# Kernel optimization log

Hardware: AMD Instinct MI355X
Metric: run time of the kernel (lower is better)

Reference implementation:

```python
import jax, jax.numpy as jnp
import numpy as np

D_MODEL = 1024
N_HEADS = 16
HEAD_DIM = D_MODEL // N_HEADS


def setup_inputs() -> dict:
    key = jax.random.key(0)
    ks = jax.random.split(key, 5)
    scale = 1.0 / np.sqrt(D_MODEL)
    return {
        "x": jax.random.normal(ks[0], (4, 2048, D_MODEL), dtype=jnp.float32),
        "W_q": jax.random.normal(ks[1], (D_MODEL, D_MODEL), dtype=jnp.float32) * scale,
        "W_k": jax.random.normal(ks[2], (D_MODEL, D_MODEL), dtype=jnp.float32) * scale,
        "W_v": jax.random.normal(ks[3], (D_MODEL, D_MODEL), dtype=jnp.float32) * scale,
        "W_o": jax.random.normal(ks[4], (D_MODEL, D_MODEL), dtype=jnp.float32) * scale,
    }


def _split_heads(t):
    # (B, T, d_model) -> (B, H, T, head_dim)
    B, T, _ = t.shape
    return t.reshape(B, T, N_HEADS, HEAD_DIM).transpose(0, 2, 1, 3)


def reference(x, W_q, W_k, W_v, W_o):
    B, T, _ = x.shape
    # torch nn.Linear: y = x @ W.T
    q = _split_heads(x @ W_q.T)
    k = _split_heads(x @ W_k.T)
    v = _split_heads(x @ W_v.T)
    scale = jnp.asarray(np.sqrt(HEAD_DIM), x.dtype)
    # (B, H, T, T) scores, additive causal mask (triu above diagonal = -inf)
    scores = jnp.einsum("bhqd,bhkd->bhqk", q, k) / scale
    causal = jnp.tril(jnp.ones((T, T), dtype=bool))
    scores = jnp.where(causal, scores, jnp.asarray(-jnp.inf, scores.dtype))
    weights = jax.nn.softmax(scores, axis=-1)
    out = jnp.einsum("bhqk,bhkd->bhqd", weights, v)
    out = out.transpose(0, 2, 1, 3).reshape(B, T, D_MODEL)
    out = out @ W_o.T
    return out, k, v
```

## Files before the change

### kernel.cpp

```cpp
#include <hip/hip_runtime.h>
#include <stdint.h>

typedef __bf16 bf16;
typedef __bf16 bf16x8 __attribute__((ext_vector_type(8)));
typedef __bf16 bf16x4 __attribute__((ext_vector_type(4)));
typedef short short4v __attribute__((ext_vector_type(4)));
typedef float f32x4 __attribute__((ext_vector_type(4)));
typedef uint32_t u32;

#define MFMA_BF16(a, b, c) __builtin_amdgcn_mfma_f32_16x16x32_bf16(a, b, c, 0, 0, 0)
#define MFMA16(a, b, c)                                                   \
  __builtin_amdgcn_mfma_f32_16x16x16bf16_1k(*(const short4v*)&(a),        \
                                            *(const short4v*)&(b), c, 0, 0, 0)

constexpr int D_MODEL = 1024;
constexpr int T_SEQ = 2048;
constexpr int NH = 16;
constexpr int HD = 64;
constexpr size_t OUT_ELEMS = (size_t)4 * T_SEQ * D_MODEL;
constexpr size_t X_ELEMS = OUT_ELEMS;
constexpr size_t W_ELEMS = (size_t)D_MODEL * D_MODEL;

__device__ __forceinline__ void gload16(const bf16* g, bf16* l) {
  __builtin_amdgcn_global_load_lds(
      (const __attribute__((address_space(1))) unsigned int*)g,
      (__attribute__((address_space(3))) unsigned int*)l, 16, 0, 0);
}

__global__ __launch_bounds__(256) void convert_kernel(
    const float* __restrict__ x, const float* __restrict__ wq,
    const float* __restrict__ wk, const float* __restrict__ wv,
    bf16* __restrict__ dst) {
  const size_t nchunk = (X_ELEMS + 3 * W_ELEMS) / 8;
  for (size_t c = (size_t)blockIdx.x * 256 + threadIdx.x; c < nchunk;
       c += (size_t)gridDim.x * 256) {
    const size_t off = c * 8;
    const float* src;
    size_t rel;
    if (off < X_ELEMS) {
      src = x;
      rel = off;
    } else {
      const size_t j = off - X_ELEMS;
      const int w = (int)(j >> 20);
      rel = j & (W_ELEMS - 1);
      src = (w == 0) ? wq : (w == 1) ? wk : wv;
    }
    const f32x4 a = *(const f32x4*)(src + rel);
    const f32x4 b = *(const f32x4*)(src + rel + 4);
    bf16x8 o;
#pragma unroll
    for (int e = 0; e < 4; ++e) {
      o[e] = (bf16)a[e];
      o[e + 4] = (bf16)b[e];
    }
    *(bf16x8*)(dst + off) = o;
  }
}

template <bool B_F32>
__global__ __launch_bounds__(256) void gemm2(
    const bf16* __restrict__ A, const bf16* __restrict__ WB,
    const float* __restrict__ WF, int modeBase, bf16* __restrict__ dstB,
    float* __restrict__ dstF1, float* __restrict__ dstF2) {
  const int z = blockIdx.z;
  const int mode = modeBase + z;
  const bf16* Bb = B_F32 ? nullptr : WB + (size_t)z * W_ELEMS;
  const int m0 = blockIdx.y * 128, n0 = blockIdx.x * 128;
  const int tid = threadIdx.x;
  const int wave = tid >> 6, lane = tid & 63;
  const int quad = lane >> 4, c16 = lane & 15;
  const int wr = wave >> 1, wc = wave & 1;

  __shared__ __align__(16) bf16 As[128 * 32];
  __shared__ __align__(16) bf16 Bs[128 * 32];

  f32x4 acc[4][4];
#pragma unroll
  for (int i = 0; i < 4; ++i)
#pragma unroll
    for (int j = 0; j < 4; ++j) acc[i][j] = (f32x4){0.f, 0.f, 0.f, 0.f};

  const int rIn = lane >> 2;
  const int kgo = (lane & 3) * 8;
  const int rA0 = wave * 16 + rIn;
  const int rA1 = (wave + 4) * 16 + rIn;

  for (int k0 = 0; k0 < 1024; k0 += 32) {
    __syncthreads();
    gload16(A + (size_t)(m0 + rA0) * 1024 + k0 + kgo, &As[wave * 512]);
    gload16(A + (size_t)(m0 + rA1) * 1024 + k0 + kgo, &As[(wave + 4) * 512]);
    if (!B_F32) {
      gload16(Bb + (size_t)(n0 + rA0) * 1024 + k0 + kgo, &Bs[wave * 512]);
      gload16(Bb + (size_t)(n0 + rA1) * 1024 + k0 + kgo, &Bs[(wave + 4) * 512]);
    } else {
#pragma unroll
      for (int p = 0; p < 2; ++p) {
        const int slot = p * 256 + tid;
        const int row = slot >> 2, kg = slot & 3;
        const float* bp = WF + (size_t)(n0 + row) * 1024 + k0 + kg * 8;
        const f32x4 b0 = *(const f32x4*)bp;
        const f32x4 b1 = *(const f32x4*)(bp + 4);
        bf16x8 vb;
#pragma unroll
        for (int e = 0; e < 4; ++e) {
          vb[e] = (bf16)b0[e];
          vb[e + 4] = (bf16)b1[e];
        }
        *(bf16x8*)&Bs[(size_t)slot * 8] = vb;
      }
    }
    asm volatile("s_waitcnt vmcnt(0)" ::: "memory");
    __syncthreads();

    const bf16x8* Av = (const bf16x8*)As;
    const bf16x8* Bv = (const bf16x8*)Bs;
    bf16x8 af[4], bfr[4];
#pragma unroll
    for (int i = 0; i < 4; ++i) af[i] = Av[(wr * 64 + i * 16 + c16) * 4 + quad];
#pragma unroll
    for (int j = 0; j < 4; ++j) bfr[j] = Bv[(wc * 64 + j * 16 + c16) * 4 + quad];
#pragma unroll
    for (int i = 0; i < 4; ++i)
#pragma unroll
      for (int j = 0; j < 4; ++j) acc[i][j] = MFMA_BF16(af[i], bfr[j], acc[i][j]);
  }

  const int row0 = m0 + wr * 64, col0 = n0 + wc * 64;
#pragma unroll
  for (int i = 0; i < 4; ++i) {
#pragma unroll
    for (int r = 0; r < 4; ++r) {
      const int row = row0 + i * 16 + quad * 4 + r;
      const int b = row >> 11, t = row & 2047;
#pragma unroll
      for (int j = 0; j < 4; ++j) {
        const int cc = col0 + j * 16 + c16;
        const float v = acc[i][j][r];
        if (mode == 0) {
          dstB[(size_t)row * 1024 + cc] = (bf16)v;
        } else if (mode == 3) {
          dstF1[(size_t)row * 1024 + cc] = v;
        } else {
          const int h = cc >> 6, d = cc & 63;
          float* df = (mode == 1) ? dstF1 : dstF2;
          df[((size_t)(b * NH + h) * T_SEQ + t) * HD + d] = v;
        }
      }
    }
  }
}

__device__ __forceinline__ void load_kv(const float* Kg, const float* Vg,
                                        int t0, int st, int sd,
                                        f32x4 pk[2][2], f32x4 pv[2][2]) {
#pragma unroll
  for (int p = 0; p < 2; ++p) {
    const float* kp = Kg + (size_t)(t0 + p * 32 + st) * HD + sd * 8;
    pk[p][0] = *(const f32x4*)kp;
    pk[p][1] = *(const f32x4*)(kp + 4);
    const float* vp = Vg + (size_t)(t0 + p * 32 + st) * HD + sd * 8;
    pv[p][0] = *(const f32x4*)vp;
    pv[p][1] = *(const f32x4*)(vp + 4);
  }
}

__global__ __launch_bounds__(256, 4) void attn_kernel(
    const bf16* __restrict__ Q, const float* __restrict__ K,
    const float* __restrict__ V, bf16* __restrict__ Aout) {
  const int bx = blockIdx.x;
  const int by = blockIdx.y;
  const int r16 = (bx + ((by >> 4) << 2)) & 15;
  const int qt = (r16 < 8) ? r16 : 23 - r16;
  const int bh = by;
  const int b = bh >> 4, h = bh & 15;
  const int tid = threadIdx.x, wave = tid >> 6, lane = tid & 63;
  const int quad = lane >> 4, c16 = lane & 15;

  __shared__ __align__(16) bf16 Ks[64 * 70];
  __shared__ __align__(16) bf16 Vs[64 * 70];

  const int q0w = qt * 128 + wave * 32;
  const bf16* Qb = Q + ((size_t)b * T_SEQ + q0w) * D_MODEL + h * HD;
  const float* Kg = K + (size_t)bh * T_SEQ * HD;
  const float* Vg = V + (size_t)bh * T_SEQ * HD;

  bf16x8 aq[2][2];
#pragma unroll
  for (int mt = 0; mt < 2; ++mt) {
    const bf16* qp = Qb + (size_t)(mt * 16 + c16) * D_MODEL + quad * 8;
    aq[mt][0] = *(const bf16x8*)qp;
    aq[mt][1] = *(const bf16x8*)(qp + 32);
  }

  f32x4 O[2][4], racc[2];
#pragma unroll
  for (int mt = 0; mt < 2; ++mt) {
    racc[mt] = (f32x4){0.f, 0.f, 0.f, 0.f};
#pragma unroll
    for (int dj = 0; dj < 4; ++dj) O[mt][dj] = (f32x4){0.f, 0.f, 0.f, 0.f};
  }

  bf16x4 ones4;
#pragma unroll
  for (int e = 0; e < 4; ++e) ones4[e] = (bf16)1.0f;

  const float sc = 0.125f * 1.44269504088896340736f;
  const int nkt = 2 * qt + 2;
  const int st = tid >> 3, sd = tid & 7;

  f32x4 pk[2][2], pv[2][2];
  load_kv(Kg, Vg, 0, st, sd, pk, pv);

  for (int kt = 0; kt < nkt; ++kt) {
    const int t0 = kt * 64;

    __syncthreads();
#pragma unroll
    for (int p = 0; p < 2; ++p) {
      const int t = p * 32 + st;
      bf16x8 kb;
#pragma unroll
      for (int e = 0; e < 4; ++e) {
        kb[e] = (bf16)pk[p][0][e];
        kb[e + 4] = (bf16)pk[p][1][e];
      }
      *(bf16x8*)&Ks[t * 70 + sd * 8] = kb;
#pragma unroll
      for (int e = 0; e < 4; ++e) {
        Vs[(sd * 8 + e) * 70 + t] = (bf16)pv[p][0][e];
        Vs[(sd * 8 + 4 + e) * 70 + t] = (bf16)pv[p][1][e];
      }
    }
    if (kt + 1 < nkt) load_kv(Kg, Vg, t0 + 64, st, sd, pk, pv);
    __syncthreads();

    const bool act[2] = {t0 <= q0w + 15, t0 <= q0w + 31};

    bf16x4 ap16[2][4];
#pragma unroll
    for (int j = 0; j < 4; ++j) {
      const bf16* kp = &Ks[(j * 16 + c16) * 70 + quad * 8];
      const bf16x8 ak0 = *(const bf16x8*)kp;
      const bf16x8 ak1 = *(const bf16x8*)(kp + 32);
#pragma unroll
      for (int mt = 0; mt < 2; ++mt) {
        if (!act[mt]) continue;
        f32x4 s = (f32x4){0.f, 0.f, 0.f, 0.f};
        s = MFMA_BF16(ak0, aq[mt][0], s);
        s = MFMA_BF16(ak1, aq[mt][1], s);
        const int trow = t0 + j * 16 + quad * 4;
        const int qcol = q0w + mt * 16 + c16;
        bf16x4 pa;
#pragma unroll
        for (int r = 0; r < 4; ++r)
          pa[r] = (bf16)((trow + r <= qcol) ? exp2f(s[r] * sc) : 0.f);
        ap16[mt][j] = pa;
      }
    }

    if (act[1]) {
#pragma unroll
      for (int mt = 0; mt < 2; ++mt) {
        if (!act[mt]) continue;
#pragma unroll
        for (int j = 0; j < 4; ++j)
          racc[mt] = MFMA16(ap16[mt][j], ones4, racc[mt]);
      }
#pragma unroll
      for (int dj = 0; dj < 4; ++dj) {
#pragma unroll
        for (int j = 0; j < 4; ++j) {
          const int a = (dj * 16 + c16) * 70 + j * 16 + quad * 4;
          bf16x4 bv;
          *(u32*)&bv = *(const u32*)&Vs[a];
          *((u32*)&bv + 1) = *(const u32*)&Vs[a + 2];
#pragma unroll
          for (int mt = 0; mt < 2; ++mt) {
            if (!act[mt]) continue;
            O[mt][dj] = MFMA16(ap16[mt][j], bv, O[mt][dj]);
          }
        }
      }
    }
  }

#pragma unroll
  for (int mt = 0; mt < 2; ++mt) {
    f32x4 inv;
#pragma unroll
    for (int r = 0; r < 4; ++r) inv[r] = 1.f / racc[mt][r];
#pragma unroll
    for (int dj = 0; dj < 4; ++dj)
#pragma unroll
      for (int r = 0; r < 4; ++r) {
        const int q = q0w + mt * 16 + quad * 4 + r;
        Aout[((size_t)b * T_SEQ + q) * D_MODEL + h * HD + dj * 16 + c16] =
            (bf16)(O[mt][dj][r] * inv[r]);
      }
  }
}

extern "C" void kernel_launch(void* const* d_in, const int* in_sizes, int n_in,
                              void* d_out, int out_size, void* d_ws, size_t ws_size,
                              hipStream_t stream) {
  const float* x = (const float*)d_in[0];
  const float* wq = (const float*)d_in[1];
  const float* wk = (const float*)d_in[2];
  const float* wv = (const float*)d_in[3];
  const float* wo = (const float*)d_in[4];

  float* out = (float*)d_out;
  float* kout = out + OUT_ELEMS;
  float* vout = out + 2 * OUT_ELEMS;

  bf16* ws = (bf16*)d_ws;
  bf16* Qbuf = ws;
  bf16* Abuf = ws;

  bf16* cvt = (bf16*)d_out;
  const bf16* xb = cvt;
  const bf16* wb = cvt + X_ELEMS;

  convert_kernel<<<dim3(2048), 256, 0, stream>>>(x, wq, wk, wv, cvt);
  gemm2<false><<<dim3(8, 64, 3), 256, 0, stream>>>(xb, wb, nullptr, 0, Qbuf,
                                                   kout, vout);
  attn_kernel<<<dim3(16, 64), 256, 0, stream>>>(Qbuf, kout, vout, Abuf);
  gemm2<true><<<dim3(8, 64, 1), 256, 0, stream>>>(Abuf, nullptr, wo, 3,
                                                  nullptr, out, nullptr);
}
```

Baseline: 436.7 us.

## Use 8 waves per attention block and pre-convert W_o to bf16

The attention kernel now runs 512 threads per block with each wave owning 16 query rows instead of 32. That halves per-wave register state and spreads the causal work more finely, while each thread loads one K/V row instead of two. Separately, W_o is converted to bf16 into the workspace when it has room, so the output projection can use the bf16-B GEMM path. The cost is an extra conversion launch, and each K/V tile is now shared by more waves.

```diff
diff --git a/kernel.cpp b/kernel.cpp
--- a/kernel.cpp
+++ b/kernel.cpp
@@ -58,6 +58,24 @@
   }
 }
 
+__global__ __launch_bounds__(256) void convert_wo(const float* __restrict__ wo,
+                                                  bf16* __restrict__ dst) {
+  const size_t nchunk = W_ELEMS / 8;
+  for (size_t c = (size_t)blockIdx.x * 256 + threadIdx.x; c < nchunk;
+       c += (size_t)gridDim.x * 256) {
+    const size_t off = c * 8;
+    const f32x4 a = *(const f32x4*)(wo + off);
+    const f32x4 b = *(const f32x4*)(wo + off + 4);
+    bf16x8 o;
+#pragma unroll
+    for (int e = 0; e < 4; ++e) {
+      o[e] = (bf16)a[e];
+      o[e + 4] = (bf16)b[e];
+    }
+    *(bf16x8*)(dst + off) = o;
+  }
+}
+
 template <bool B_F32>
 __global__ __launch_bounds__(256) void gemm2(
     const bf16* __restrict__ A, const bf16* __restrict__ WB,
@@ -152,54 +170,45 @@
 }
 
 __device__ __forceinline__ void load_kv(const float* Kg, const float* Vg,
-                                        int t0, int st, int sd,
-                                        f32x4 pk[2][2], f32x4 pv[2][2]) {
-#pragma unroll
-  for (int p = 0; p < 2; ++p) {
-    const float* kp = Kg + (size_t)(t0 + p * 32 + st) * HD + sd * 8;
-    pk[p][0] = *(const f32x4*)kp;
-    pk[p][1] = *(const f32x4*)(kp + 4);
-    const float* vp = Vg + (size_t)(t0 + p * 32 + st) * HD + sd * 8;
-    pv[p][0] = *(const f32x4*)vp;
-    pv[p][1] = *(const f32x4*)(vp + 4);
-  }
-}
-
-__global__ __launch_bounds__(256, 4) void attn_kernel(
+                                        int t0, int st, int sd, f32x4 pk[2],
+                                        f32x4 pv[2]) {
+  const float* kp = Kg + (size_t)(t0 + st) * HD + sd * 8;
+  pk[0] = *(const f32x4*)kp;
+  pk[1] = *(const f32x4*)(kp + 4);
+  const float* vp = Vg + (size_t)(t0 + st) * HD + sd * 8;
+  pv[0] = *(const f32x4*)vp;
+  pv[1] = *(const f32x4*)(vp + 4);
+}
+
+__global__ __launch_bounds__(512, 8) void attn_kernel(
     const bf16* __restrict__ Q, const float* __restrict__ K,
     const float* __restrict__ V, bf16* __restrict__ Aout) {
   const int bx = blockIdx.x;
   const int by = blockIdx.y;
   const int r16 = (bx + ((by >> 4) << 2)) & 15;
   const int qt = (r16 < 8) ? r16 : 23 - r16;
-  const int bh = by;
-  const int b = bh >> 4, h = bh & 15;
+  const int b = by >> 4, h = by & 15;
   const int tid = threadIdx.x, wave = tid >> 6, lane = tid & 63;
   const int quad = lane >> 4, c16 = lane & 15;
 
   __shared__ __align__(16) bf16 Ks[64 * 70];
   __shared__ __align__(16) bf16 Vs[64 * 70];
 
-  const int q0w = qt * 128 + wave * 32;
+  const int q0w = qt * 128 + wave * 16;
   const bf16* Qb = Q + ((size_t)b * T_SEQ + q0w) * D_MODEL + h * HD;
-  const float* Kg = K + (size_t)bh * T_SEQ * HD;
-  const float* Vg = V + (size_t)bh * T_SEQ * HD;
-
-  bf16x8 aq[2][2];
-#pragma unroll
-  for (int mt = 0; mt < 2; ++mt) {
-    const bf16* qp = Qb + (size_t)(mt * 16 + c16) * D_MODEL + quad * 8;
-    aq[mt][0] = *(const bf16x8*)qp;
-    aq[mt][1] = *(const bf16x8*)(qp + 32);
-  }
-
-  f32x4 O[2][4], racc[2];
-#pragma unroll
-  for (int mt = 0; mt < 2; ++mt) {
-    racc[mt] = (f32x4){0.f, 0.f, 0.f, 0.f};
-#pragma unroll
-    for (int dj = 0; dj < 4; ++dj) O[mt][dj] = (f32x4){0.f, 0.f, 0.f, 0.f};
-  }
+  const float* Kg = K + (size_t)by * T_SEQ * HD;
+  const float* Vg = V + (size_t)by * T_SEQ * HD;
+
+  bf16x8 aq[2];
+  {
+    const bf16* qp = Qb + (size_t)c16 * D_MODEL + quad * 8;
+    aq[0] = *(const bf16x8*)qp;
+    aq[1] = *(const bf16x8*)(qp + 32);
+  }
+
+  f32x4 O[4], racc = (f32x4){0.f, 0.f, 0.f, 0.f};
+#pragma unroll
+  for (int dj = 0; dj < 4; ++dj) O[dj] = (f32x4){0.f, 0.f, 0.f, 0.f};
 
   bf16x4 ones4;
 #pragma unroll
@@ -209,64 +218,52 @@
   const int nkt = 2 * qt + 2;
   const int st = tid >> 3, sd = tid & 7;
 
-  f32x4 pk[2][2], pv[2][2];
+  f32x4 pk[2], pv[2];
   load_kv(Kg, Vg, 0, st, sd, pk, pv);
 
   for (int kt = 0; kt < nkt; ++kt) {
     const int t0 = kt * 64;
 
     __syncthreads();
-#pragma unroll
-    for (int p = 0; p < 2; ++p) {
-      const int t = p * 32 + st;
+    {
       bf16x8 kb;
 #pragma unroll
       for (int e = 0; e < 4; ++e) {
-        kb[e] = (bf16)pk[p][0][e];
-        kb[e + 4] = (bf16)pk[p][1][e];
-      }
-      *(bf16x8*)&Ks[t * 70 + sd * 8] = kb;
+        kb[e] = (bf16)pk[0][e];
+        kb[e + 4] = (bf16)pk[1][e];
+      }
+      *(bf16x8*)&Ks[st * 70 + sd * 8] = kb;
 #pragma unroll
       for (int e = 0; e < 4; ++e) {
-        Vs[(sd * 8 + e) * 70 + t] = (bf16)pv[p][0][e];
-        Vs[(sd * 8 + 4 + e) * 70 + t] = (bf16)pv[p][1][e];
+        Vs[(sd * 8 + e) * 70 + st] = (bf16)pv[0][e];
+        Vs[(sd * 8 + 4 + e) * 70 + st] = (bf16)pv[1][e];
       }
     }
     if (kt + 1 < nkt) load_kv(Kg, Vg, t0 + 64, st, sd, pk, pv);
     __syncthreads();
 
-    const bool act[2] = {t0 <= q0w + 15, t0 <= q0w + 31};
-
-    bf16x4 ap16[2][4];
-#pragma unroll
-    for (int j = 0; j < 4; ++j) {
-      const bf16* kp = &Ks[(j * 16 + c16) * 70 + quad * 8];
-      const bf16x8 ak0 = *(const bf16x8*)kp;
-      const bf16x8 ak1 = *(const bf16x8*)(kp + 32);
-#pragma unroll
-      for (int mt = 0; mt < 2; ++mt) {
-        if (!act[mt]) continue;
+    const bool act = t0 <= q0w + 15;
+
+    bf16x4 ap16[4];
+    if (act) {
+#pragma unroll
+      for (int j = 0; j < 4; ++j) {
+        const bf16* kp = &Ks[(j * 16 + c16) * 70 + quad * 8];
+        const bf16x8 ak0 = *(const bf16x8*)kp;
+        const bf16x8 ak1 = *(const bf16x8*)(kp + 32);
         f32x4 s = (f32x4){0.f, 0.f, 0.f, 0.f};
-        s = MFMA_BF16(ak0, aq[mt][0], s);
-        s = MFMA_BF16(ak1, aq[mt][1], s);
+        s = MFMA_BF16(ak0, aq[0], s);
+        s = MFMA_BF16(ak1, aq[1], s);
         const int trow = t0 + j * 16 + quad * 4;
-        const int qcol = q0w + mt * 16 + c16;
+        const int qcol = q0w + c16;
         bf16x4 pa;
 #pragma unroll
         for (int r = 0; r < 4; ++r)
           pa[r] = (bf16)((trow + r <= qcol) ? exp2f(s[r] * sc) : 0.f);
-        ap16[mt][j] = pa;
-      }
-    }
-
-    if (act[1]) {
-#pragma unroll
-      for (int mt = 0; mt < 2; ++mt) {
-        if (!act[mt]) continue;
-#pragma unroll
-        for (int j = 0; j < 4; ++j)
-          racc[mt] = MFMA16(ap16[mt][j], ones4, racc[mt]);
-      }
+        ap16[j] = pa;
+      }
+#pragma unroll
+      for (int j = 0; j < 4; ++j) racc = MFMA16(ap16[j], ones4, racc);
 #pragma unroll
       for (int dj = 0; dj < 4; ++dj) {
 #pragma unroll
@@ -275,30 +272,23 @@
           bf16x4 bv;
           *(u32*)&bv = *(const u32*)&Vs[a];
           *((u32*)&bv + 1) = *(const u32*)&Vs[a + 2];
-#pragma unroll
-          for (int mt = 0; mt < 2; ++mt) {
-            if (!act[mt]) continue;
-            O[mt][dj] = MFMA16(ap16[mt][j], bv, O[mt][dj]);
-          }
+          O[dj] = MFMA16(ap16[j], bv, O[dj]);
         }
       }
     }
   }
 
-#pragma unroll
-  for (int mt = 0; mt < 2; ++mt) {
-    f32x4 inv;
-#pragma unroll
-    for (int r = 0; r < 4; ++r) inv[r] = 1.f / racc[mt][r];
-#pragma unroll
-    for (int dj = 0; dj < 4; ++dj)
-#pragma unroll
-      for (int r = 0; r < 4; ++r) {
-        const int q = q0w + mt * 16 + quad * 4 + r;
-        Aout[((size_t)b * T_SEQ + q) * D_MODEL + h * HD + dj * 16 + c16] =
-            (bf16)(O[mt][dj][r] * inv[r]);
-      }
-  }
+  f32x4 inv;
+#pragma unroll
+  for (int r = 0; r < 4; ++r) inv[r] = 1.f / racc[r];
+#pragma unroll
+  for (int dj = 0; dj < 4; ++dj)
+#pragma unroll
+    for (int r = 0; r < 4; ++r) {
+      const int q = q0w + quad * 4 + r;
+      Aout[((size_t)b * T_SEQ + q) * D_MODEL + h * HD + dj * 16 + c16] =
+          (bf16)(O[dj][r] * inv[r]);
+    }
 }
 
 extern "C" void kernel_launch(void* const* d_in, const int* in_sizes, int n_in,
@@ -322,10 +312,19 @@
   const bf16* xb = cvt;
   const bf16* wb = cvt + X_ELEMS;
 
+  const bool wo_bf = ws_size >= (X_ELEMS + W_ELEMS) * sizeof(bf16);
+  bf16* wo_b = ws + X_ELEMS;
+
   convert_kernel<<<dim3(2048), 256, 0, stream>>>(x, wq, wk, wv, cvt);
+  if (wo_bf) convert_wo<<<dim3(512), 256, 0, stream>>>(wo, wo_b);
   gemm2<false><<<dim3(8, 64, 3), 256, 0, stream>>>(xb, wb, nullptr, 0, Qbuf,
                                                    kout, vout);
-  attn_kernel<<<dim3(16, 64), 256, 0, stream>>>(Qbuf, kout, vout, Abuf);
-  gemm2<true><<<dim3(8, 64, 1), 256, 0, stream>>>(Abuf, nullptr, wo, 3,
-                                                  nullptr, out, nullptr);
-}
+  attn_kernel<<<dim3(16, 64), 512, 0, stream>>>(Qbuf, kout, vout, Abuf);
+  if (wo_bf) {
+    gemm2<false><<<dim3(8, 64, 1), 256, 0, stream>>>(Abuf, wo_b, nullptr, 3,
+                                                     nullptr, out, nullptr);
+  } else {
+    gemm2<true><<<dim3(8, 64, 1), 256, 0, stream>>>(Abuf, nullptr, wo, 3,
+                                                    nullptr, out, nullptr);
+  }
+}
```

Measured after the change: 499.4 us. 1.14x slower.

## Use ds_read_b64_tr_b16 for V operand and pre-convert W_o to bf16

Applied to the files above, without the earlier changes.

The V tile is now stored in LDS in a 16x16-blocked row layout with vectorized 16-byte writes, replacing scalar transposed stores. The PV MFMA B operands are read with the hardware transpose-read instruction ds_read_b64_tr_b16. A separate kernel converts W_o to bf16 in workspace so the output projection can use the bf16-B GEMM path instead of converting fp32 weights inside the GEMM. This adds an extra launch and relies on the workspace being large enough; it falls back to the old path otherwise.

```diff
diff --git a/kernel.cpp b/kernel.cpp
--- a/kernel.cpp
+++ b/kernel.cpp
@@ -6,12 +6,18 @@
 typedef __bf16 bf16x4 __attribute__((ext_vector_type(4)));
 typedef short short4v __attribute__((ext_vector_type(4)));
 typedef float f32x4 __attribute__((ext_vector_type(4)));
+typedef int v2i __attribute__((ext_vector_type(2)));
 typedef uint32_t u32;
 
 #define MFMA_BF16(a, b, c) __builtin_amdgcn_mfma_f32_16x16x32_bf16(a, b, c, 0, 0, 0)
 #define MFMA16(a, b, c)                                                   \
   __builtin_amdgcn_mfma_f32_16x16x16bf16_1k(*(const short4v*)&(a),        \
                                             *(const short4v*)&(b), c, 0, 0, 0)
+
+#define TRREAD(dst, va, IMM)                                             \
+  asm volatile("ds_read_b64_tr_b16 %0, %1 offset:" #IMM                  \
+               : "=v"(dst)                                               \
+               : "v"(va))
 
 constexpr int D_MODEL = 1024;
 constexpr int T_SEQ = 2048;
@@ -58,6 +64,24 @@
   }
 }
 
+__global__ __launch_bounds__(256) void convert_wo(const float* __restrict__ wo,
+                                                  bf16* __restrict__ dst) {
+  const size_t nchunk = W_ELEMS / 8;
+  for (size_t c = (size_t)blockIdx.x * 256 + threadIdx.x; c < nchunk;
+       c += (size_t)gridDim.x * 256) {
+    const size_t off = c * 8;
+    const f32x4 a = *(const f32x4*)(wo + off);
+    const f32x4 b = *(const f32x4*)(wo + off + 4);
+    bf16x8 o;
+#pragma unroll
+    for (int e = 0; e < 4; ++e) {
+      o[e] = (bf16)a[e];
+      o[e + 4] = (bf16)b[e];
+    }
+    *(bf16x8*)(dst + off) = o;
+  }
+}
+
 template <bool B_F32>
 __global__ __launch_bounds__(256) void gemm2(
     const bf16* __restrict__ A, const bf16* __restrict__ WB,
@@ -172,18 +196,17 @@
   const int by = blockIdx.y;
   const int r16 = (bx + ((by >> 4) << 2)) & 15;
   const int qt = (r16 < 8) ? r16 : 23 - r16;
-  const int bh = by;
-  const int b = bh >> 4, h = bh & 15;
+  const int b = by >> 4, h = by & 15;
   const int tid = threadIdx.x, wave = tid >> 6, lane = tid & 63;
   const int quad = lane >> 4, c16 = lane & 15;
 
   __shared__ __align__(16) bf16 Ks[64 * 70];
-  __shared__ __align__(16) bf16 Vs[64 * 70];
+  __shared__ __align__(16) bf16 Vs[4096];
 
   const int q0w = qt * 128 + wave * 32;
   const bf16* Qb = Q + ((size_t)b * T_SEQ + q0w) * D_MODEL + h * HD;
-  const float* Kg = K + (size_t)bh * T_SEQ * HD;
-  const float* Vg = V + (size_t)bh * T_SEQ * HD;
+  const float* Kg = K + (size_t)by * T_SEQ * HD;
+  const float* Vg = V + (size_t)by * T_SEQ * HD;
 
   bf16x8 aq[2][2];
 #pragma unroll
@@ -208,6 +231,9 @@
   const float sc = 0.125f * 1.44269504088896340736f;
   const int nkt = 2 * qt + 2;
   const int st = tid >> 3, sd = tid & 7;
+  const u32 vtr =
+      (u32)(uintptr_t)(const __attribute__((address_space(3))) bf16*)Vs +
+      (u32)lane * 8;
 
   f32x4 pk[2][2], pv[2][2];
   load_kv(Kg, Vg, 0, st, sd, pk, pv);
@@ -219,18 +245,17 @@
 #pragma unroll
     for (int p = 0; p < 2; ++p) {
       const int t = p * 32 + st;
-      bf16x8 kb;
+      bf16x8 kb, vb;
 #pragma unroll
       for (int e = 0; e < 4; ++e) {
         kb[e] = (bf16)pk[p][0][e];
         kb[e + 4] = (bf16)pk[p][1][e];
+        vb[e] = (bf16)pv[p][0][e];
+        vb[e + 4] = (bf16)pv[p][1][e];
       }
       *(bf16x8*)&Ks[t * 70 + sd * 8] = kb;
-#pragma unroll
-      for (int e = 0; e < 4; ++e) {
-        Vs[(sd * 8 + e) * 70 + t] = (bf16)pv[p][0][e];
-        Vs[(sd * 8 + 4 + e) * 70 + t] = (bf16)pv[p][1][e];
-      }
+      *(bf16x8*)&Vs[(((t >> 4) * 4 + (sd >> 1)) * 256) + (t & 15) * 16 +
+                    (sd & 1) * 8] = vb;
     }
     if (kt + 1 < nkt) load_kv(Kg, Vg, t0 + 64, st, sd, pk, pv);
     __syncthreads();
@@ -267,21 +292,29 @@
         for (int j = 0; j < 4; ++j)
           racc[mt] = MFMA16(ap16[mt][j], ones4, racc[mt]);
       }
-#pragma unroll
-      for (int dj = 0; dj < 4; ++dj) {
-#pragma unroll
-        for (int j = 0; j < 4; ++j) {
-          const int a = (dj * 16 + c16) * 70 + j * 16 + quad * 4;
-          bf16x4 bv;
-          *(u32*)&bv = *(const u32*)&Vs[a];
-          *((u32*)&bv + 1) = *(const u32*)&Vs[a + 2];
-#pragma unroll
-          for (int mt = 0; mt < 2; ++mt) {
-            if (!act[mt]) continue;
-            O[mt][dj] = MFMA16(ap16[mt][j], bv, O[mt][dj]);
-          }
-        }
-      }
+      v2i bv0, bv1, bv2, bv3;
+#define PV_DJ(DJ, O0, O1, O2, O3)                                        \
+  {                                                                      \
+    TRREAD(bv0, vtr, O0);                                                \
+    TRREAD(bv1, vtr, O1);                                                \
+    TRREAD(bv2, vtr, O2);                                                \
+    TRREAD(bv3, vtr, O3);                                                \
+    asm volatile("s_waitcnt lgkmcnt(0)" ::: "memory");                   \
+    __builtin_amdgcn_sched_barrier(0);                                   \
+    _Pragma("unroll") for (int mt = 0; mt < 2; ++mt) {                   \
+      if (act[mt]) {                                                     \
+        O[mt][DJ] = MFMA16(ap16[mt][0], bv0, O[mt][DJ]);                 \
+        O[mt][DJ] = MFMA16(ap16[mt][1], bv1, O[mt][DJ]);                 \
+        O[mt][DJ] = MFMA16(ap16[mt][2], bv2, O[mt][DJ]);                 \
+        O[mt][DJ] = MFMA16(ap16[mt][3], bv3, O[mt][DJ]);                 \
+      }                                                                  \
+    }                                                                    \
+  }
+      PV_DJ(0, 0, 2048, 4096, 6144)
+      PV_DJ(1, 512, 2560, 4608, 6656)
+      PV_DJ(2, 1024, 3072, 5120, 7168)
+      PV_DJ(3, 1536, 3584, 5632, 7680)
+#undef PV_DJ
     }
   }
 
@@ -322,10 +355,19 @@
   const bf16* xb = cvt;
   const bf16* wb = cvt + X_ELEMS;
 
+  const bool wo_bf = ws_size >= (X_ELEMS + W_ELEMS) * sizeof(bf16);
+  bf16* wo_b = ws + X_ELEMS;
+
   convert_kernel<<<dim3(2048), 256, 0, stream>>>(x, wq, wk, wv, cvt);
+  if (wo_bf) convert_wo<<<dim3(512), 256, 0, stream>>>(wo, wo_b);
   gemm2<false><<<dim3(8, 64, 3), 256, 0, stream>>>(xb, wb, nullptr, 0, Qbuf,
                                                    kout, vout);
   attn_kernel<<<dim3(16, 64), 256, 0, stream>>>(Qbuf, kout, vout, Abuf);
-  gemm2<true><<<dim3(8, 64, 1), 256, 0, stream>>>(Abuf, nullptr, wo, 3,
-                                                  nullptr, out, nullptr);
-}
+  if (wo_bf) {
+    gemm2<false><<<dim3(8, 64, 1), 256, 0, stream>>>(Abuf, wo_b, nullptr, 3,
+                                                     nullptr, out, nullptr);
+  } else {
+    gemm2<true><<<dim3(8, 64, 1), 256, 0, stream>>>(Abuf, nullptr, wo, 3,
+                                                    nullptr, out, nullptr);
+  }
+}
```

Result: faster. 388.8 us (-11.0%).
